# Optimization experiments

Measured on AMD Instinct MI355X. Metric: run time of the kernel, lower is better.

The kernel has to match this reference:

```python
import jax, jax.numpy as jnp
import numpy as np

N_FFT = 256
WINDOW_OUT = 64
N_BINS = N_FFT // 2 + 1  # 129


def _irfft_matrices(n_fft, window_out):
    n = n_fft // 2 + 1
    m_real = np.fft.irfft(np.eye(n), n=n_fft)          # [n, n_fft]
    m_imag = np.fft.irfft(1j * np.eye(n), n=n_fft)     # [n, n_fft]
    m_real = m_real[:, -window_out:]                   # truncate to last window_out samples
    m_imag = m_imag[:, -window_out:]
    return (jnp.asarray(m_real, dtype=jnp.float32), jnp.asarray(m_imag, dtype=jnp.float32))


def setup_inputs() -> dict:
    key = jax.random.key(0)
    k1, k2 = jax.random.split(key)
    re = jax.random.normal(k1, (64, 4000, N_BINS), dtype=jnp.float32)
    im = jax.random.normal(k2, (64, 4000, N_BINS), dtype=jnp.float32)
    m_real, m_imag = _irfft_matrices(N_FFT, WINDOW_OUT)
    return {"re": re, "im": im, "m_real": m_real, "m_imag": m_imag}


def reference(re, im, m_real, m_imag):
    # Dense IRFFT: out = re @ M_real + im @ M_imag, fused add of the two matmul outputs.
    # re, im: [B, T, n_bins]; m_real, m_imag: [n_bins, window_out] -> out: [B, T, window_out]
    return jnp.einsum('btn,no->bto', re, m_real) + jnp.einsum('btn,no->bto', im, m_imag)
```

## Files before the change

kernel.cpp:

```cpp
#include <hip/hip_runtime.h>
#include <hip/hip_bf16.h>

typedef __bf16 bf8 __attribute__((ext_vector_type(8)));
typedef float f32x4 __attribute__((ext_vector_type(4)));

#define NBINS 129
#define ROWS_IT 16
#define ITERS 16
#define MATB 8192
#define BUFB (2 * MATB)

__device__ __forceinline__ void gload_lds16(const float* src, char* ldsdst) {
    __builtin_amdgcn_global_load_lds(
        (const __attribute__((address_space(1))) void*)src,
        (__attribute__((address_space(3))) void*)ldsdst, 16, 0, 0);
}

__global__ __launch_bounds__(256, 4)
void irfft_mm(const float* __restrict__ re,
              const float* __restrict__ im,
              const float* __restrict__ mr,
              const float* __restrict__ mi,
              float* __restrict__ out)
{
    __shared__ __align__(16) char lds[2][BUFB];

    const int tid  = threadIdx.x;
    const int lane = tid & 63;
    const int w    = tid >> 6;
    const int r16  = lane & 15;
    const int q    = lane >> 4;
    const int rk   = r16 & 7;

    const int blockrow = blockIdx.x * (ROWS_IT * ITERS);

    const int    smat  = w >> 1;
    const int    srow0 = (w & 1) * 8;
    const float* ssrc  = smat ? im : re;
    const int    lrow  = lane >> 5;
    const int    p     = lane & 31;

    float trr[2], tri[2];

    {
        char* b0 = lds[0];
        #pragma unroll
        for (int i = 0; i < 4; ++i) {
            const int trow = srow0 + 2 * i + lrow;
            const int g    = p ^ (trow & 7);
            gload_lds16(ssrc + (long)(blockrow + trow) * NBINS + g * 4,
                        b0 + smat * MATB + (srow0 + 2 * i) * 512 + lane * 16);
        }
        trr[0] = re[(long)(blockrow + r16) * NBINS + 128];
        tri[0] = im[(long)(blockrow + r16) * NBINS + 128];
    }

    bf8 afr[2][4];
    #pragma unroll
    for (int m = 0; m < 2; ++m) {
        const float* M = m ? mi : mr;
        #pragma unroll
        for (int t = 0; t < 4; ++t) {
            bf8 a;
            #pragma unroll
            for (int j = 0; j < 8; ++j)
                a[j] = (__bf16)M[(t * 32 + q * 8 + j) * 64 + w * 16 + r16];
            afr[m][t] = a;
        }
    }
    const f32x4 mt0 = *(const f32x4*)(mr + 128 * 64 + w * 16 + q * 4);
    const f32x4 mt1 = *(const f32x4*)(mi + 128 * 64 + w * 16 + q * 4);

    #pragma unroll
    for (int it = 0; it < ITERS; ++it) {
        char* bufc = lds[it & 1];
        const int rowbase = blockrow + it * ROWS_IT;

        __builtin_amdgcn_sched_barrier(0);
        asm volatile("s_waitcnt vmcnt(0)" ::: "memory");
        __builtin_amdgcn_s_barrier();
        __builtin_amdgcn_sched_barrier(0);

        if (it + 1 < ITERS) {
            char* bn = lds[(it + 1) & 1];
            const int rbn = rowbase + ROWS_IT;
            #pragma unroll
            for (int i = 0; i < 4; ++i) {
                const int trow = srow0 + 2 * i + lrow;
                const int g    = p ^ (trow & 7);
                gload_lds16(ssrc + (long)(rbn + trow) * NBINS + g * 4,
                            bn + smat * MATB + (srow0 + 2 * i) * 512 + lane * 16);
            }
            trr[(it + 1) & 1] = re[(long)(rbn + r16) * NBINS + 128];
            tri[(it + 1) & 1] = im[(long)(rbn + r16) * NBINS + 128];
        }

        f32x4 acc = {0.0f, 0.0f, 0.0f, 0.0f};
        #pragma unroll
        for (int m = 0; m < 2; ++m) {
            const char* mb = bufc + m * MATB + r16 * 512;
            #pragma unroll
            for (int t = 0; t < 4; ++t) {
                const int j0 = t * 8 + q * 2;
                const f32x4 lo = *(const f32x4*)(mb + ((j0)     ^ rk) * 16);
                const f32x4 hi = *(const f32x4*)(mb + ((j0 + 1) ^ rk) * 16);
                bf8 bfr;
                #pragma unroll
                for (int jj = 0; jj < 4; ++jj) {
                    bfr[jj]     = (__bf16)lo[jj];
                    bfr[4 + jj] = (__bf16)hi[jj];
                }
                acc = __builtin_amdgcn_mfma_f32_16x16x32_bf16(afr[m][t], bfr, acc, 0, 0, 0);
            }
            const float xt = m ? tri[it & 1] : trr[it & 1];
            const f32x4 mt = m ? mt1 : mt0;
            #pragma unroll
            for (int jj = 0; jj < 4; ++jj) acc[jj] += xt * mt[jj];
        }

        *(f32x4*)(out + (long)(rowbase + r16) * 64 + w * 16 + q * 4) = acc;
    }
}

extern "C" void kernel_launch(void* const* d_in, const int* in_sizes, int n_in,
                              void* d_out, int out_size, void* d_ws, size_t ws_size,
                              hipStream_t stream)
{
    const float* re = (const float*)d_in[0];
    const float* im = (const float*)d_in[1];
    const float* mr = (const float*)d_in[2];
    const float* mi = (const float*)d_in[3];
    float* out = (float*)d_out;

    const long rows = (long)in_sizes[0] / NBINS;
    const int grid = (int)(rows / (ROWS_IT * ITERS));
    irfft_mm<<<grid, 256, 0, stream>>>(re, im, mr, mi, out);
}
```

Baseline: 71.86 us.

## Triple-buffer LDS staging with prefetch distance two and stage tail bin via LDS

Result: faster. 68.02 us (-5.3%).

```diff
diff --git a/kernel.cpp b/kernel.cpp
--- a/kernel.cpp
+++ b/kernel.cpp
@@ -8,7 +8,8 @@
 #define ROWS_IT 16
 #define ITERS 16
 #define MATB 8192
-#define BUFB (2 * MATB)
+#define TAILB 512
+#define BUFB (2 * MATB + TAILB)
 
 __device__ __forceinline__ void gload_lds16(const float* src, char* ldsdst) {
     __builtin_amdgcn_global_load_lds(
@@ -16,14 +17,14 @@
         (__attribute__((address_space(3))) void*)ldsdst, 16, 0, 0);
 }
 
-__global__ __launch_bounds__(256, 4)
+__global__ __launch_bounds__(256, 3)
 void irfft_mm(const float* __restrict__ re,
               const float* __restrict__ im,
               const float* __restrict__ mr,
               const float* __restrict__ mi,
               float* __restrict__ out)
 {
-    __shared__ __align__(16) char lds[2][BUFB];
+    __shared__ __align__(16) char lds[3][BUFB];
 
     const int tid  = threadIdx.x;
     const int lane = tid & 63;
@@ -32,7 +33,7 @@
     const int q    = lane >> 4;
     const int rk   = r16 & 7;
 
-    const int blockrow = blockIdx.x * (ROWS_IT * ITERS);
+    const long blockrow = (long)blockIdx.x * (ROWS_IT * ITERS);
 
     const int    smat  = w >> 1;
     const int    srow0 = (w & 1) * 8;
@@ -40,20 +41,24 @@
     const int    lrow  = lane >> 5;
     const int    p     = lane & 31;
 
-    float trr[2], tri[2];
+    #define STAGE(bn, rbn)                                                        \
+        {                                                                         \
+            char* _b = (bn);                                                      \
+            const long _r = (rbn);                                                \
+            _Pragma("unroll")                                                     \
+            for (int i = 0; i < 4; ++i) {                                         \
+                const int trow = srow0 + 2 * i + lrow;                            \
+                const int g    = p ^ (trow & 7);   \
+                gload_lds16(ssrc + (_r + trow) * (long)NBINS + g * 4,             \
+                            _b + smat * MATB + (srow0 + 2 * i) * 512 + lane * 16);\
+            }                                                                     \
+            if (lane < 8)      \
+                gload_lds16(ssrc + (_r + srow0 + lane) * (long)NBINS + 128,       \
+                            _b + 2 * MATB + smat * 256 + (srow0 + lane) * 16);    \
+        }
 
-    {
-        char* b0 = lds[0];
-        #pragma unroll
-        for (int i = 0; i < 4; ++i) {
-            const int trow = srow0 + 2 * i + lrow;
-            const int g    = p ^ (trow & 7);
-            gload_lds16(ssrc + (long)(blockrow + trow) * NBINS + g * 4,
-                        b0 + smat * MATB + (srow0 + 2 * i) * 512 + lane * 16);
-        }
-        trr[0] = re[(long)(blockrow + r16) * NBINS + 128];
-        tri[0] = im[(long)(blockrow + r16) * NBINS + 128];
-    }
+    STAGE(lds[0], blockrow);
+    STAGE(lds[1], blockrow + ROWS_IT);
 
     bf8 afr[2][4];
     #pragma unroll
@@ -73,27 +78,17 @@
 
     #pragma unroll
     for (int it = 0; it < ITERS; ++it) {
-        char* bufc = lds[it & 1];
-        const int rowbase = blockrow + it * ROWS_IT;
+        char* bufc = lds[it % 3];
+        const long rowbase = blockrow + it * ROWS_IT;
 
         __builtin_amdgcn_sched_barrier(0);
-        asm volatile("s_waitcnt vmcnt(0)" ::: "memory");
+        if (it < ITERS - 1) asm volatile("s_waitcnt vmcnt(5)" ::: "memory");
+        else                asm volatile("s_waitcnt vmcnt(0)" ::: "memory");
         __builtin_amdgcn_s_barrier();
         __builtin_amdgcn_sched_barrier(0);
 
-        if (it + 1 < ITERS) {
-            char* bn = lds[(it + 1) & 1];
-            const int rbn = rowbase + ROWS_IT;
-            #pragma unroll
-            for (int i = 0; i < 4; ++i) {
-                const int trow = srow0 + 2 * i + lrow;
-                const int g    = p ^ (trow & 7);
-                gload_lds16(ssrc + (long)(rbn + trow) * NBINS + g * 4,
-                            bn + smat * MATB + (srow0 + 2 * i) * 512 + lane * 16);
-            }
-            trr[(it + 1) & 1] = re[(long)(rbn + r16) * NBINS + 128];
-            tri[(it + 1) & 1] = im[(long)(rbn + r16) * NBINS + 128];
-        }
+        if (it + 2 < ITERS)
+            STAGE(lds[(it + 2) % 3], rowbase + 2 * ROWS_IT);
 
         f32x4 acc = {0.0f, 0.0f, 0.0f, 0.0f};
         #pragma unroll
@@ -112,14 +107,15 @@
                 }
                 acc = __builtin_amdgcn_mfma_f32_16x16x32_bf16(afr[m][t], bfr, acc, 0, 0, 0);
             }
-            const float xt = m ? tri[it & 1] : trr[it & 1];
+            const float xt = *(const float*)(bufc + 2 * MATB + m * 256 + r16 * 16);
             const f32x4 mt = m ? mt1 : mt0;
             #pragma unroll
             for (int jj = 0; jj < 4; ++jj) acc[jj] += xt * mt[jj];
         }
 
-        *(f32x4*)(out + (long)(rowbase + r16) * 64 + w * 16 + q * 4) = acc;
+        *(f32x4*)(out + (rowbase + r16) * 64 + w * 16 + q * 4) = acc;
     }
+    #undef STAGE
 }
 
 extern "C" void kernel_launch(void* const* d_in, const int* in_sizes, int n_in,
```
